# Kernel optimization log

Measured on AMD Instinct MI355X. Metric: run time of the kernel, lower is better.

## Reference

```python
import jax, jax.numpy as jnp
import numpy as np

EMB = 2048
HEADS = 16
HEAD_DIM = EMB // HEADS
MIN_WINDOW = 64
MAX_WINDOW = 256
ROPE_BASE = 10000.0


def setup_inputs() -> dict:
    key = jax.random.key(0)
    ks = jax.random.split(key, 5)
    B, S = 2, 2048
    x = jax.random.normal(ks[0], (B, S, EMB), dtype=jnp.float32)
    w_qkv = jax.random.normal(ks[1], (3 * EMB, EMB), dtype=jnp.float32) * (EMB ** -0.5)
    w_out = jax.random.normal(ks[2], (EMB, EMB), dtype=jnp.float32) * (EMB ** -0.5)
    w_c1 = jax.random.normal(ks[3], (EMB // 4, EMB), dtype=jnp.float32) * 0.1 * (EMB ** -0.5)
    w_c2 = jax.random.normal(ks[4], (1, EMB // 4), dtype=jnp.float32) * 0.1 * ((EMB // 4) ** -0.5)
    return {"x": x, "w_qkv": w_qkv, "w_out": w_out, "w_c1": w_c1, "w_c2": w_c2}


def _rotate_half(t):
    # interleaved pairs: [-x1, x0, -x3, x2, ...]
    x1 = t[..., ::2]
    x2 = t[..., 1::2]
    return jnp.stack((-x2, x1), axis=-1).reshape(t.shape)


def _rope_tables(seq_len, dtype):
    inv_freq = 1.0 / (ROPE_BASE ** (jnp.arange(0, HEAD_DIM, 2, dtype=jnp.float32) / HEAD_DIM))
    pos = jnp.arange(seq_len, dtype=jnp.float32)
    freqs = jnp.outer(pos, inv_freq)                      # [S, D/2]
    emb = jnp.concatenate([freqs, freqs], axis=-1)        # [S, D]
    return jnp.cos(emb)[None, None].astype(dtype), jnp.sin(emb)[None, None].astype(dtype)


def _forward(x, w_qkv, w_out, w_c1, w_c2):
    B, S, _ = x.shape
    scale = HEAD_DIM ** -0.5

    qkv = x @ w_qkv.T                                     # [B, S, 3E]
    qkv = qkv.reshape(B, S, 3, HEADS, HEAD_DIM).transpose(2, 0, 3, 1, 4)
    q, k, v = qkv[0], qkv[1], qkv[2]                      # each [B, H, S, D]

    cos, sin = _rope_tables(S, x.dtype)
    q = q * cos + _rotate_half(q) * sin
    k = k * cos + _rotate_half(k) * sin

    scores = jnp.einsum("bhqd,bhkd->bhqk", q, k) * scale  # [B, H, S, S]

    # adaptive window size from input complexity
    var = jnp.var(x.reshape(B, -1), axis=1, ddof=1)        # torch unbiased var over dims [1,2]
    var_norm = jax.nn.sigmoid(var * 10.0 - 5.0)
    x_mean = x.mean(axis=1)                                # [B, E]
    hidden = jax.nn.silu(x_mean @ w_c1.T)
    learned = jax.nn.sigmoid(hidden @ w_c2.T)[:, 0]        # [B]
    complexity = (var_norm + learned) / 2.0
    window_f = MIN_WINDOW + complexity * (MAX_WINDOW - MIN_WINDOW)
    window = window_f.mean().astype(jnp.int32)             # trunc like .int()
    window = jnp.maximum(jnp.minimum(window, S), MIN_WINDOW)

    # causal + sliding-window mask: keep 0 <= q_pos - k_pos < window
    pos = jnp.arange(S)
    rel = pos[:, None] - pos[None, :]                      # [S, S]
    keep = (rel >= 0) & (rel < window)
    scores = jnp.where(keep[None, None], scores, -jnp.inf)

    attn = jax.nn.softmax(scores, axis=-1)
    out = jnp.einsum("bhqk,bhkd->bhqd", attn, v)           # [B, H, S, D]
    out = out.transpose(0, 2, 1, 3).reshape(B, S, EMB)
    return out @ w_out.T


def reference(x, w_qkv, w_out, w_c1, w_c2):
    return _forward(x, w_qkv, w_out, w_c1, w_c2)
```

## Files before the change

kernel.cpp:

```cpp
#include <hip/hip_runtime.h>
#include <math.h>


#define S_LEN 2048
#define EMB 2048
#define HEADS 16
#define HDIM 128
#define NT 20
#define PSTR 336

typedef _Float16 f16x8 __attribute__((ext_vector_type(8)));
typedef _Float16 f16x4 __attribute__((ext_vector_type(4)));
typedef float f32x4 __attribute__((ext_vector_type(4)));

__device__ __forceinline__ void gld16(const void* g, void* l) {
    __builtin_amdgcn_global_load_lds(
        (const __attribute__((address_space(1))) unsigned int*)g,
        (__attribute__((address_space(3))) unsigned int*)l, 16, 0, 0);
}

__global__ void rope_table(float2* __restrict__ cstab) {
    int s = blockIdx.x;
    int d = threadIdx.x;
    int j = d & 63;
    double inv = pow(10000.0, -(double)j / 64.0);
    double ang = (double)s * inv;
    cstab[s * HDIM + d] = make_float2((float)cos(ang), (float)sin(ang));
}

__global__ __launch_bounds__(256) void col_reduce(const float* __restrict__ x,
                                                  float* __restrict__ xmean_acc,
                                                  double* __restrict__ scal,
                                                  _Float16* __restrict__ x16) {
    int b = blockIdx.z;
    int cg = blockIdx.x;
    int sg = blockIdx.y;
    int e = cg * 256 + threadIdx.x;
    const size_t base = ((size_t)b * S_LEN + sg * 32) * EMB;
    const float* xb = x + base;
    _Float16* xo = x16 + base;
    double csum = 0.0, csq = 0.0;
    for (int s = 0; s < 32; ++s) {
        float v = xb[(size_t)s * EMB + e];
        xo[(size_t)s * EMB + e] = (_Float16)v;
        csum += v;
        csq += (double)v * (double)v;
    }
    atomicAdd(xmean_acc + b * EMB + e, (float)csum);
    __shared__ double rs[256], rq[256];
    rs[threadIdx.x] = csum; rq[threadIdx.x] = csq;
    __syncthreads();
    for (int off = 128; off > 0; off >>= 1) {
        if (threadIdx.x < off) {
            rs[threadIdx.x] += rs[threadIdx.x + off];
            rq[threadIdx.x] += rq[threadIdx.x + off];
        }
        __syncthreads();
    }
    if (threadIdx.x == 0) {
        atomicAdd(&scal[b], rs[0]);
        atomicAdd(&scal[2 + b], rq[0]);
    }
}

__global__ __launch_bounds__(256) void hidden_kernel(const float* __restrict__ xmean_acc,
                                                     const float* __restrict__ wc1,
                                                     float* __restrict__ hidden) {
    int j = blockIdx.x;
    int b = blockIdx.y;
    const float* xm = xmean_acc + b * EMB;
    const float* wr = wc1 + (size_t)j * EMB;
    double acc = 0.0;
    for (int k = threadIdx.x; k < EMB; k += 256)
        acc += (double)xm[k] * (double)wr[k];
    __shared__ double red[256];
    red[threadIdx.x] = acc;
    __syncthreads();
    for (int off = 128; off > 0; off >>= 1) {
        if (threadIdx.x < off) red[threadIdx.x] += red[threadIdx.x + off];
        __syncthreads();
    }
    if (threadIdx.x == 0) {
        double z = red[0] * (1.0 / 2048.0);
        hidden[b * 512 + j] = (float)(z / (1.0 + exp(-z)));
    }
}

__global__ __launch_bounds__(512) void window_kernel(const float* __restrict__ hidden,
                                                     const float* __restrict__ wc2,
                                                     const double* __restrict__ scal,
                                                     int* __restrict__ wout) {
    __shared__ double red[512];
    __shared__ double wfs[2];
    for (int b = 0; b < 2; ++b) {
        red[threadIdx.x] = (double)hidden[b * 512 + threadIdx.x] * (double)wc2[threadIdx.x];
        __syncthreads();
        for (int off = 256; off > 0; off >>= 1) {
            if (threadIdx.x < off) red[threadIdx.x] += red[threadIdx.x + off];
            __syncthreads();
        }
        if (threadIdx.x == 0) {
            double pre = red[0];
            double learned = 1.0 / (1.0 + exp(-pre));
            const double N = (double)S_LEN * (double)EMB;
            double sum = scal[b], sq = scal[2 + b];
            double var = (sq - sum * sum / N) / (N - 1.0);
            double vn = 1.0 / (1.0 + exp(-(var * 10.0 - 5.0)));
            double comp = 0.5 * (vn + learned);
            wfs[b] = 64.0 + comp * 192.0;
        }
        __syncthreads();
    }
    if (threadIdx.x == 0) {
        float wf = (float)(0.5 * (wfs[0] + wfs[1]));
        int w = (int)wf;
        if (w > S_LEN) w = S_LEN;
        if (w < 64) w = 64;
        *wout = w;
    }
}

__global__ __launch_bounds__(256) void cvt_f16(const float* __restrict__ s,
                                               _Float16* __restrict__ d, int n4) {
    int i = blockIdx.x * 256 + threadIdx.x;
    if (i < n4) {
        float4 v = ((const float4*)s)[i];
        f16x4 o;
        o.x = (_Float16)v.x; o.y = (_Float16)v.y;
        o.z = (_Float16)v.z; o.w = (_Float16)v.w;
        ((f16x4*)d)[i] = o;
    }
}

#define GEMM_PROLOGUE(An, Wn)                                                   \
    __shared__ _Float16 As[128 * 32];                                           \
    __shared__ _Float16 Bs[128 * 32];                                           \
    const int tid = threadIdx.x;                                                \
    const int lane = tid & 63;                                                  \
    const int wv = tid >> 6;                                                    \
    const int wm = wv >> 1, wn = wv & 1;                                        \
    const int m0 = blockIdx.y * 128;                                            \
    const int n0 = blockIdx.x * 128;                                            \
    const int srow = wv * 32 + (lane >> 2);                                     \
    const int schunk = (lane & 3) ^ ((lane >> 3) & 3);     \
    const int scol = schunk * 8;                                                \
    const _Float16* agp = An + (size_t)(m0 + srow) * EMB + scol;                \
    const _Float16* bgp = Wn + (size_t)(n0 + srow) * EMB + scol;                \
    _Float16* al = &As[(wv * 32) * 32];                                         \
    _Float16* bl = &Bs[(wv * 32) * 32];                                         \
    const int frow = lane & 15;                                                 \
    const int fcol = ((lane >> 4) ^ ((frow >> 1) & 3)) * 8;      \
    f32x4 acc[4][4] = {};                                                       \
    for (int k0 = 0; k0 < EMB; k0 += 32) {                                      \
        __syncthreads();                                                        \
        gld16(agp, al);                                                         \
        gld16(agp + 16 * EMB, al + 16 * 32);                                    \
        gld16(bgp, bl);                                                         \
        gld16(bgp + 16 * EMB, bl + 16 * 32);                                    \
        agp += 32; bgp += 32;                                                   \
        __syncthreads();                                                        \
        f16x8 af[4], bf[4];                                                     \
        _Pragma("unroll")                                                       \
        for (int i = 0; i < 4; ++i)                                             \
            af[i] = *(const f16x8*)&As[(wm * 64 + i * 16 + frow) * 32 + fcol];  \
        _Pragma("unroll")                                                       \
        for (int j = 0; j < 4; ++j)                                             \
            bf[j] = *(const f16x8*)&Bs[(wn * 64 + j * 16 + frow) * 32 + fcol];  \
        _Pragma("unroll")                                                       \
        for (int i = 0; i < 4; ++i)                                             \
            _Pragma("unroll")                                                   \
            for (int j = 0; j < 4; ++j)                                         \
                acc[i][j] = __builtin_amdgcn_mfma_f32_16x16x32_f16(             \
                    af[i], bf[j], acc[i][j], 0, 0, 0);                          \
    }                                                                           \
    const int colbase = lane & 15;                                              \
    const int rowoff = (lane >> 4) * 4;

__global__ __launch_bounds__(256) void gemm_qkv_f16(const _Float16* __restrict__ An,
                                                    const _Float16* __restrict__ Wn,
                                                    _Float16* __restrict__ q16,
                                                    _Float16* __restrict__ k16,
                                                    _Float16* __restrict__ vt,
                                                    const float2* __restrict__ cstab) {
    GEMM_PROLOGUE(An, Wn)
    const int which = n0 >> 11;
    const int h = (n0 >> 7) & 15;
    if (which == 2) {
#pragma unroll
        for (int i = 0; i < 4; ++i) {
#pragma unroll
            for (int j = 0; j < 4; ++j) {
                const int d = wn * 64 + j * 16 + colbase;
                int m = m0 + wm * 64 + i * 16 + rowoff;
                int b = m >> 11, s = m & 2047;
                f16x4 o;
#pragma unroll
                for (int r = 0; r < 4; ++r) o[r] = (_Float16)acc[i][j][r];
                *(f16x4*)&vt[(((size_t)b * HEADS + h) * HDIM + d) * S_LEN + s] = o;
            }
        }
    } else {
        _Float16* dst = which == 0 ? q16 : k16;
        const float sgn = (colbase & 1) ? 1.f : -1.f;
#pragma unroll
        for (int i = 0; i < 4; ++i) {
#pragma unroll
            for (int j = 0; j < 4; ++j) {
                const int d = wn * 64 + j * 16 + colbase;
#pragma unroll
                for (int r = 0; r < 4; ++r) {
                    int m = m0 + wm * 64 + i * 16 + rowoff + r;
                    int b = m >> 11, s = m & 2047;
                    float a = acc[i][j][r];
                    float p = __shfl_xor(a, 1, 64);
                    float2 cs = cstab[(size_t)s * HDIM + d];
                    float o = fmaf(a, cs.x, sgn * p * cs.y);
                    dst[(((size_t)b * HEADS + h) * S_LEN + s) * HDIM + d] = (_Float16)o;
                }
            }
        }
    }
}

__global__ __launch_bounds__(256) void gemm_out_f16(const _Float16* __restrict__ An,
                                                    const _Float16* __restrict__ Wn,
                                                    float* __restrict__ C) {
    GEMM_PROLOGUE(An, Wn)
#pragma unroll
    for (int i = 0; i < 4; ++i) {
#pragma unroll
        for (int j = 0; j < 4; ++j) {
            const int n = n0 + wn * 64 + j * 16 + colbase;
#pragma unroll
            for (int r = 0; r < 4; ++r) {
                int m = m0 + wm * 64 + i * 16 + rowoff + r;
                C[(size_t)m * EMB + n] = acc[i][j][r];
            }
        }
    }
}

__global__ __launch_bounds__(256) void attn_mfma(const _Float16* __restrict__ q16,
                                                 const _Float16* __restrict__ k16,
                                                 const _Float16* __restrict__ v16t,
                                                 _Float16* __restrict__ ob,
                                                 const int* __restrict__ wptr) {
    const int q0 = blockIdx.x * 64;
    const int h = blockIdx.y;
    const int b = blockIdx.z;
    const int tid = threadIdx.x;
    const int lane = tid & 63;
    const int wv = tid >> 6;
    const int w = *wptr;

    __shared__ _Float16 Pl[4][16 * PSTR];
    _Float16* Pw = Pl[wv];

    const int kstart = q0 - 256;
    int ntlo_w = (257 - w) >> 4;
    int ntlo_n = q0 < 256 ? ((256 - q0) >> 4) : 0;
    const int ntlo = ntlo_w > ntlo_n ? ntlo_w : ntlo_n;

    const int frow = lane & 15;
    const int fgrp = lane >> 4;
    const int fcol = fgrp * 8;

    const size_t bh = (size_t)b * HEADS + h;
    const _Float16* Qp = q16 + (bh * S_LEN + q0 + wv * 16 + frow) * HDIM + fcol;
    const _Float16* Kb = k16 + bh * S_LEN * HDIM;
    const _Float16* Vt = v16t + bh * HDIM * S_LEN;

    f16x8 aq[4];
#pragma unroll
    for (int ks = 0; ks < 4; ++ks) aq[ks] = *(const f16x8*)(Qp + ks * 32);

    f32x4 accs[NT];
#pragma unroll
    for (int nt = 0; nt < NT; ++nt) accs[nt] = (f32x4){0.f, 0.f, 0.f, 0.f};
#pragma unroll
    for (int nt = 0; nt < NT; ++nt) {
        if (nt < ntlo) continue;
        int krow = kstart + nt * 16 + frow;
        if (krow < 0) krow = 0;
        const _Float16* kp = Kb + (size_t)krow * HDIM + fcol;
#pragma unroll
        for (int ks = 0; ks < 4; ++ks) {
            f16x8 bk = *(const f16x8*)(kp + ks * 32);
            accs[nt] = __builtin_amdgcn_mfma_f32_16x16x32_f16(aq[ks], bk, accs[nt], 0, 0, 0);
        }
    }

    const int qrow = fgrp * 4;
    const int qabs = q0 + wv * 16 + qrow;
    const float scale = 0.08838834764831845f;
    float mx[4] = {-INFINITY, -INFINITY, -INFINITY, -INFINITY};
#pragma unroll
    for (int nt = 0; nt < NT; ++nt) {
        int key = kstart + nt * 16 + frow;
#pragma unroll
        for (int r = 0; r < 4; ++r) {
            int rel = (qabs + r) - key;
            bool keep = (key >= 0) && (rel >= 0) && (rel < w);
            float s = keep ? accs[nt][r] * scale : -INFINITY;
            accs[nt][r] = s;
            mx[r] = fmaxf(mx[r], s);
        }
    }
#pragma unroll
    for (int r = 0; r < 4; ++r) {
        float m = mx[r];
#pragma unroll
        for (int off = 1; off < 16; off <<= 1)
            m = fmaxf(m, __shfl_xor(m, off, 64));
        mx[r] = m;
    }

    float ls[4] = {0.f, 0.f, 0.f, 0.f};
#pragma unroll
    for (int nt = 0; nt < NT; ++nt) {
#pragma unroll
        for (int r = 0; r < 4; ++r) {
            float p = __expf(accs[nt][r] - mx[r]);
            ls[r] += p;
            Pw[(qrow + r) * PSTR + nt * 16 + frow] = (_Float16)p;
        }
    }
    float inv[4];
#pragma unroll
    for (int r = 0; r < 4; ++r) {
        float l = ls[r];
#pragma unroll
        for (int off = 1; off < 16; off <<= 1)
            l += __shfl_xor(l, off, 64);
        inv[r] = 1.f / l;
    }

    const int pvlo = ntlo >> 1;
    f32x4 acco[8];
#pragma unroll
    for (int jt = 0; jt < 8; ++jt) acco[jt] = (f32x4){0.f, 0.f, 0.f, 0.f};
    const _Float16* Pr = &Pl[wv][frow * PSTR];
#pragma unroll
    for (int kp = 0; kp < 10; ++kp) {
        if (kp < pvlo) continue;
        f16x8 ap = *(const f16x8*)(Pr + kp * 32 + fcol);
        int kv = kstart + kp * 32 + fcol;
        if (kv < 0) kv = 0;
#pragma unroll
        for (int jt = 0; jt < 8; ++jt) {
            f16x8 bv = *(const f16x8*)(Vt + (size_t)(jt * 16 + frow) * S_LEN + kv);
            acco[jt] = __builtin_amdgcn_mfma_f32_16x16x32_f16(ap, bv, acco[jt], 0, 0, 0);
        }
    }

#pragma unroll
    for (int jt = 0; jt < 8; ++jt) {
#pragma unroll
        for (int r = 0; r < 4; ++r) {
            int s = qabs + r;
            ob[((size_t)b * S_LEN + s) * EMB + h * HDIM + jt * 16 + frow] =
                (_Float16)(acco[jt][r] * inv[r]);
        }
    }
}

extern "C" void kernel_launch(void* const* d_in, const int* in_sizes, int n_in,
                              void* d_out, int out_size, void* d_ws, size_t ws_size,
                              hipStream_t stream) {
    const float* x     = (const float*)d_in[0];
    const float* w_qkv = (const float*)d_in[1];
    const float* w_out = (const float*)d_in[2];
    const float* w_c1  = (const float*)d_in[3];
    const float* w_c2  = (const float*)d_in[4];
    float* out = (float*)d_out;
    char* ws = (char*)d_ws;

    double*    scal   = (double*)(ws + 0);
    int*       win    = (int*)(ws + 64);
    float*     xmean  = (float*)(ws + 128);
    float*     hidden = (float*)(ws + 16640);
    float2*    cstab  = (float2*)(ws + 32768);
    _Float16*  x16    = (_Float16*)(ws + 4194304);
    _Float16*  wqkv16 = (_Float16*)(ws + 20971520);
    _Float16*  ao16   = (_Float16*)(ws + 20971520);
    _Float16*  v16t   = (_Float16*)(ws + 46137344);
    _Float16*  q16    = (_Float16*)(ws + 62914560);
    _Float16*  k16    = (_Float16*)(ws + 79691776);
    _Float16*  wout16 = (_Float16*)(ws + 96468992);

    hipMemsetAsync(d_ws, 0, 32768, stream);

    rope_table<<<dim3(S_LEN), dim3(HDIM), 0, stream>>>(cstab);
    col_reduce<<<dim3(8, 64, 2), dim3(256), 0, stream>>>(x, xmean, scal, x16);
    hidden_kernel<<<dim3(512, 2), dim3(256), 0, stream>>>(xmean, w_c1, hidden);
    window_kernel<<<dim3(1), dim3(512), 0, stream>>>(hidden, w_c2, scal, win);

    cvt_f16<<<dim3(12288), dim3(256), 0, stream>>>(w_qkv, wqkv16, 3145728);
    cvt_f16<<<dim3(4096), dim3(256), 0, stream>>>(w_out, wout16, 1048576);

    gemm_qkv_f16<<<dim3(48, 32), dim3(256), 0, stream>>>(x16, wqkv16, q16, k16, v16t, cstab);
    attn_mfma<<<dim3(32, HEADS, 2), dim3(256), 0, stream>>>(q16, k16, v16t, ao16, win);
    gemm_out_f16<<<dim3(16, 32), dim3(256), 0, stream>>>(ao16, wout16, out);
}
```

Baseline: 458.3 us.

## Double GEMM k-tile to 64, vectorize col_reduce, merge weight conversion kernels

The shared GEMM prologue now stages 64-wide k tiles with an 8-chunk XOR swizzle and runs two MFMA sub-steps per barrier pair, halving loop iterations and synchronisations. col_reduce reads float4 and writes f16x4 per thread with four column accumulators, so it launches with a quarter of the blocks. The two weight fp32-to-fp16 conversion launches are merged into one kernel. LDS per block doubles, which may reduce occupancy for the GEMMs.

After: 406.4 us. 1.13x faster.

```diff
diff --git a/kernel.cpp b/kernel.cpp
--- a/kernel.cpp
+++ b/kernel.cpp
@@ -35,20 +35,30 @@
     int b = blockIdx.z;
     int cg = blockIdx.x;
     int sg = blockIdx.y;
-    int e = cg * 256 + threadIdx.x;
+    int e4 = cg * 256 + threadIdx.x;
     const size_t base = ((size_t)b * S_LEN + sg * 32) * EMB;
-    const float* xb = x + base;
-    _Float16* xo = x16 + base;
-    double csum = 0.0, csq = 0.0;
+    const float4* xb = (const float4*)(x + base) + e4;
+    f16x4* xo = (f16x4*)(x16 + base) + e4;
+    double cs0 = 0.0, cs1 = 0.0, cs2 = 0.0, cs3 = 0.0;
+    double cq = 0.0;
     for (int s = 0; s < 32; ++s) {
-        float v = xb[(size_t)s * EMB + e];
-        xo[(size_t)s * EMB + e] = (_Float16)v;
-        csum += v;
-        csq += (double)v * (double)v;
-    }
-    atomicAdd(xmean_acc + b * EMB + e, (float)csum);
+        float4 v = xb[(size_t)s * (EMB / 4)];
+        f16x4 o;
+        o.x = (_Float16)v.x; o.y = (_Float16)v.y;
+        o.z = (_Float16)v.z; o.w = (_Float16)v.w;
+        xo[(size_t)s * (EMB / 4)] = o;
+        cs0 += v.x; cs1 += v.y; cs2 += v.z; cs3 += v.w;
+        cq += (double)v.x * v.x + (double)v.y * v.y +
+              (double)v.z * v.z + (double)v.w * v.w;
+    }
+    float* xm = xmean_acc + b * EMB + e4 * 4;
+    atomicAdd(xm + 0, (float)cs0);
+    atomicAdd(xm + 1, (float)cs1);
+    atomicAdd(xm + 2, (float)cs2);
+    atomicAdd(xm + 3, (float)cs3);
     __shared__ double rs[256], rq[256];
-    rs[threadIdx.x] = csum; rq[threadIdx.x] = csq;
+    rs[threadIdx.x] = cs0 + cs1 + cs2 + cs3;
+    rq[threadIdx.x] = cq;
     __syncthreads();
     for (int off = 128; off > 0; off >>= 1) {
         if (threadIdx.x < off) {
@@ -120,58 +130,75 @@
     }
 }
 
-__global__ __launch_bounds__(256) void cvt_f16(const float* __restrict__ s,
-                                               _Float16* __restrict__ d, int n4) {
+#define NQKV4 3145728
+#define NOUT4 1048576
+__global__ __launch_bounds__(256) void cvt_weights(const float* __restrict__ wqkv,
+                                                   const float* __restrict__ wout,
+                                                   _Float16* __restrict__ d_qkv,
+                                                   _Float16* __restrict__ d_out) {
     int i = blockIdx.x * 256 + threadIdx.x;
-    if (i < n4) {
-        float4 v = ((const float4*)s)[i];
-        f16x4 o;
-        o.x = (_Float16)v.x; o.y = (_Float16)v.y;
-        o.z = (_Float16)v.z; o.w = (_Float16)v.w;
-        ((f16x4*)d)[i] = o;
-    }
+    const float4* s;
+    f16x4* d;
+    if (i < NQKV4) {
+        s = (const float4*)wqkv + i;
+        d = (f16x4*)d_qkv + i;
+    } else {
+        s = (const float4*)wout + (i - NQKV4);
+        d = (f16x4*)d_out + (i - NQKV4);
+    }
+    float4 v = *s;
+    f16x4 o;
+    o.x = (_Float16)v.x; o.y = (_Float16)v.y;
+    o.z = (_Float16)v.z; o.w = (_Float16)v.w;
+    *d = o;
 }
 
 #define GEMM_PROLOGUE(An, Wn)                                                   \
-    __shared__ _Float16 As[128 * 32];                                           \
-    __shared__ _Float16 Bs[128 * 32];                                           \
+    __shared__ _Float16 As[128 * 64];                                           \
+    __shared__ _Float16 Bs[128 * 64];                                           \
     const int tid = threadIdx.x;                                                \
     const int lane = tid & 63;                                                  \
     const int wv = tid >> 6;                                                    \
     const int wm = wv >> 1, wn = wv & 1;                                        \
     const int m0 = blockIdx.y * 128;                                            \
     const int n0 = blockIdx.x * 128;                                            \
-    const int srow = wv * 32 + (lane >> 2);                                     \
-    const int schunk = (lane & 3) ^ ((lane >> 3) & 3);     \
-    const int scol = schunk * 8;                                                \
-    const _Float16* agp = An + (size_t)(m0 + srow) * EMB + scol;                \
-    const _Float16* bgp = Wn + (size_t)(n0 + srow) * EMB + scol;                \
-    _Float16* al = &As[(wv * 32) * 32];                                         \
-    _Float16* bl = &Bs[(wv * 32) * 32];                                         \
+    const int lrow = lane >> 3;                                       \
+    const int lchk = (lane & 7) ^ lrow;                       \
+    const int srow = wv * 32 + lrow;                                            \
+    const _Float16* agp = An + (size_t)(m0 + srow) * EMB + lchk * 8;            \
+    const _Float16* bgp = Wn + (size_t)(n0 + srow) * EMB + lchk * 8;            \
+    _Float16* al = &As[wv * 32 * 64];                                           \
+    _Float16* bl = &Bs[wv * 32 * 64];                                           \
     const int frow = lane & 15;                                                 \
-    const int fcol = ((lane >> 4) ^ ((frow >> 1) & 3)) * 8;      \
+    const int fgrp = lane >> 4;                                                 \
     f32x4 acc[4][4] = {};                                                       \
-    for (int k0 = 0; k0 < EMB; k0 += 32) {                                      \
+    for (int k0 = 0; k0 < EMB; k0 += 64) {                                      \
         __syncthreads();                                                        \
-        gld16(agp, al);                                                         \
-        gld16(agp + 16 * EMB, al + 16 * 32);                                    \
-        gld16(bgp, bl);                                                         \
-        gld16(bgp + 16 * EMB, bl + 16 * 32);                                    \
-        agp += 32; bgp += 32;                                                   \
+        _Pragma("unroll")                                                       \
+        for (int t = 0; t < 4; ++t) {                                           \
+            gld16(agp + (size_t)t * 8 * EMB, al + t * 8 * 64);                  \
+            gld16(bgp + (size_t)t * 8 * EMB, bl + t * 8 * 64);                  \
+        }                                                                       \
+        agp += 64; bgp += 64;                                                   \
         __syncthreads();                                                        \
-        f16x8 af[4], bf[4];                                                     \
         _Pragma("unroll")                                                       \
-        for (int i = 0; i < 4; ++i)                                             \
-            af[i] = *(const f16x8*)&As[(wm * 64 + i * 16 + frow) * 32 + fcol];  \
-        _Pragma("unroll")                                                       \
-        for (int j = 0; j < 4; ++j)                                             \
-            bf[j] = *(const f16x8*)&Bs[(wn * 64 + j * 16 + frow) * 32 + fcol];  \
-        _Pragma("unroll")                                                       \
-        for (int i = 0; i < 4; ++i)                                             \
+        for (int ks = 0; ks < 2; ++ks) {                                        \
+            f16x8 af[4], bf[4];                                                 \
+            _Pragma("unroll")                                                   \
+            for (int i = 0; i < 4; ++i)                                         \
+                af[i] = *(const f16x8*)&As[(wm * 64 + i * 16 + frow) * 64 +     \
+                                           (((ks * 4 + fgrp) ^ (frow & 7)) * 8)]; \
             _Pragma("unroll")                                                   \
             for (int j = 0; j < 4; ++j)                                         \
-                acc[i][j] = __builtin_amdgcn_mfma_f32_16x16x32_f16(             \
-                    af[i], bf[j], acc[i][j], 0, 0, 0);                          \
+                bf[j] = *(const f16x8*)&Bs[(wn * 64 + j * 16 + frow) * 64 +     \
+                                           (((ks * 4 + fgrp) ^ (frow & 7)) * 8)]; \
+            _Pragma("unroll")                                                   \
+            for (int i = 0; i < 4; ++i)                                         \
+                _Pragma("unroll")                                               \
+                for (int j = 0; j < 4; ++j)                                     \
+                    acc[i][j] = __builtin_amdgcn_mfma_f32_16x16x32_f16(         \
+                        af[i], bf[j], acc[i][j], 0, 0, 0);                      \
+        }                                                                       \
     }                                                                           \
     const int colbase = lane & 15;                                              \
     const int rowoff = (lane >> 4) * 4;
@@ -391,12 +418,12 @@
     hipMemsetAsync(d_ws, 0, 32768, stream);
 
     rope_table<<<dim3(S_LEN), dim3(HDIM), 0, stream>>>(cstab);
-    col_reduce<<<dim3(8, 64, 2), dim3(256), 0, stream>>>(x, xmean, scal, x16);
+    col_reduce<<<dim3(2, 64, 2), dim3(256), 0, stream>>>(x, xmean, scal, x16);
     hidden_kernel<<<dim3(512, 2), dim3(256), 0, stream>>>(xmean, w_c1, hidden);
     window_kernel<<<dim3(1), dim3(512), 0, stream>>>(hidden, w_c2, scal, win);
 
-    cvt_f16<<<dim3(12288), dim3(256), 0, stream>>>(w_qkv, wqkv16, 3145728);
-    cvt_f16<<<dim3(4096), dim3(256), 0, stream>>>(w_out, wout16, 1048576);
+    cvt_weights<<<dim3((NQKV4 + NOUT4) / 256), dim3(256), 0, stream>>>(
+        w_qkv, w_out, wqkv16, wout16);
 
     gemm_qkv_f16<<<dim3(48, 32), dim3(256), 0, stream>>>(x16, wqkv16, q16, k16, v16t, cstab);
     attn_mfma<<<dim3(32, HEADS, 2), dim3(256), 0, stream>>>(q16, k16, v16t, ao16, win);
```
